# Performance work log

Hardware: AMD Instinct MI355X
Metric: run time of the kernel (lower is better)

Reference implementation:

```python
import jax, jax.numpy as jnp
import numpy as np

N_NODES = 50000
N_EDGES = 800000
IN_CH = 128
EDGE_DIM = 32
H1, H2, H3, OUT = 128, 64, 32, 1


def _linear_params(key, fan_in, fan_out, bias=True):
    k1, k2 = jax.random.split(key)
    scale = 1.0 / np.sqrt(fan_in)
    W = jax.random.uniform(k1, (fan_in, fan_out), jnp.float32, -scale, scale)
    if bias:
        b = jax.random.uniform(k2, (fan_out,), jnp.float32, -scale, scale)
        return W, b
    return W


def setup_inputs() -> dict:
    key = jax.random.key(0)
    ks = jax.random.split(key, 32)
    inp = {
        'x': jax.random.normal(ks[0], (N_NODES, IN_CH), jnp.float32),
        'edge_index': jax.random.randint(ks[1], (2, N_EDGES), 0, N_NODES, jnp.int64),
        'edge_attr': jax.random.normal(ks[2], (N_EDGES, EDGE_DIM), jnp.float32),
    }
    dims = [(IN_CH, H1), (H1, H2), (H2, H3)]
    ki = 3
    for l, (fi, fo) in enumerate(dims, start=1):
        inp[f'Wq{l}'], inp[f'bq{l}'] = _linear_params(ks[ki], fi, fo); ki += 1
        inp[f'Wk{l}'], inp[f'bk{l}'] = _linear_params(ks[ki], fi, fo); ki += 1
        inp[f'Wv{l}'], inp[f'bv{l}'] = _linear_params(ks[ki], fi, fo); ki += 1
        inp[f'We{l}'] = _linear_params(ks[ki], EDGE_DIM, fo, bias=False); ki += 1
        inp[f'Ws{l}'], inp[f'bs{l}'] = _linear_params(ks[ki], fi, fo); ki += 1
    inp['Wc'], inp['bc'] = _linear_params(ks[ki], H3, OUT)
    return inp


def _tconv(x, src, dst, edge_attr, Wq, bq, Wk, bk, Wv, bv, We, Ws, bs):
    # TransformerConv, heads=1: edge-conditioned attention with segment softmax over dst
    q = x @ Wq + bq                      # [N, d]
    k = x @ Wk + bk                      # [N, d]
    v = x @ Wv + bv                      # [N, d]
    e = edge_attr @ We                   # [E, d]
    k_e = k[src] + e                     # gather + edge key
    v_e = v[src] + e                     # gather + edge value
    d = q.shape[-1]
    alpha = jnp.sum(q[dst] * k_e, axis=-1) / jnp.sqrt(jnp.asarray(d, x.dtype))  # [E]
    m = jax.ops.segment_max(alpha, dst, num_segments=N_NODES)
    a = jnp.exp(alpha - m[dst])
    s = jax.ops.segment_sum(a, dst, num_segments=N_NODES)
    a = a / s[dst]
    agg = jax.ops.segment_sum(a[:, None] * v_e, dst, num_segments=N_NODES)
    return agg + x @ Ws + bs             # root/skip connection


def reference(x, edge_index, edge_attr,
              Wq1, bq1, Wk1, bk1, Wv1, bv1, We1, Ws1, bs1,
              Wq2, bq2, Wk2, bk2, Wv2, bv2, We2, Ws2, bs2,
              Wq3, bq3, Wk3, bk3, Wv3, bv3, We3, Ws3, bs3,
              Wc, bc):
    src, dst = edge_index[0], edge_index[1]
    h = jax.nn.relu(_tconv(x, src, dst, edge_attr, Wq1, bq1, Wk1, bk1, Wv1, bv1, We1, Ws1, bs1))
    h = jax.nn.relu(_tconv(h, src, dst, edge_attr, Wq2, bq2, Wk2, bk2, Wv2, bv2, We2, Ws2, bs2))
    h = jax.nn.relu(_tconv(h, src, dst, edge_attr, Wq3, bq3, Wk3, bk3, Wv3, bv3, We3, Ws3, bs3))
    return h @ Wc + bc
```

## Files before the change

### kernel.cpp

```cpp
#include <hip/hip_runtime.h>
#include <math.h>

#define N_NODES 50000
#define N_EDGES 800000

typedef __bf16 bf16;
typedef __bf16 bf16x8 __attribute__((ext_vector_type(8)));
typedef float f32x4 __attribute__((ext_vector_type(4)));

__device__ __forceinline__ float bflo(unsigned r) {
  union { unsigned u; float f; } c; c.u = r << 16; return c.f;
}
__device__ __forceinline__ float bfhi(unsigned r) {
  union { unsigned u; float f; } c; c.u = r & 0xffff0000u; return c.f;
}

__global__ void k_detect(const int* ei, int* flags) {
  if (threadIdx.x == 0 && blockIdx.x == 0) {
    int is64 = 1;
    for (int i = 0; i < 128; ++i) {
      if (ei[2 * i + 1] != 0) { is64 = 0; break; }
    }
    flags[0] = is64;
  }
}

__device__ __forceinline__ int load_idx(const int* ei, int e, int is64, int which) {
  size_t idx = (size_t)which * N_EDGES + (size_t)e;
  return is64 ? ei[2 * idx] : ei[idx];
}


__global__ void k_zero(int* p, int n) {
  int i = blockIdx.x * blockDim.x + threadIdx.x;
  if (i < n) p[i] = 0;
}

__global__ void k_hist(const int* ei, const int* flags, int* counts) {
  int e = blockIdx.x * blockDim.x + threadIdx.x;
  int is64 = flags[0];
  if (e < N_EDGES) {
    int dst = load_idx(ei, e, is64, 1);
    if (dst >= 0 && dst < N_NODES) atomicAdd(&counts[dst], 1);
  }
}

__global__ void k_scan1(const int* counts, int* row_ptr, int* bsum) {
  __shared__ int buf[1024];
  int t = threadIdx.x;
  int i = blockIdx.x * 1024 + t;
  int v = (i < N_NODES) ? counts[i] : 0;
  buf[t] = v;
  __syncthreads();
  for (int off = 1; off < 1024; off <<= 1) {
    int x = (t >= off) ? buf[t - off] : 0;
    __syncthreads();
    buf[t] += x;
    __syncthreads();
  }
  if (i < N_NODES) row_ptr[i] = buf[t] - v;
  if (t == 1023) bsum[blockIdx.x] = buf[1023];
}

__global__ void k_scan2(int* bsum, int* row_ptr) {
  constexpr int NB = (N_NODES + 1023) / 1024;
  int t = threadIdx.x;
  int v = (t < NB) ? bsum[t] : 0;
  int inc = v;
#pragma unroll
  for (int off = 1; off < 64; off <<= 1) {
    int x = __shfl_up(inc, off, 64);
    if (t >= off) inc += x;
  }
  if (t < NB) bsum[t] = inc - v;
  if (t == 63) row_ptr[N_NODES] = inc;
}

__global__ void k_scan3(const int* bsum, int* row_ptr, int* cursor) {
  int i = blockIdx.x * 1024 + threadIdx.x;
  if (i < N_NODES) {
    int r = row_ptr[i] + bsum[blockIdx.x];
    row_ptr[i] = r;
    cursor[i] = r;
  }
}

__global__ void k_scatter(const int* ei, const int* flags, int* cursor,
                          int* csr_src, int* csr_eid) {
  int e = blockIdx.x * blockDim.x + threadIdx.x;
  int is64 = flags[0];
  if (e < N_EDGES) {
    int src = load_idx(ei, e, is64, 0);
    int dst = load_idx(ei, e, is64, 1);
    if (dst >= 0 && dst < N_NODES && src >= 0 && src < N_NODES) {
      int pos = atomicAdd(&cursor[dst], 1);
      if (pos >= 0 && pos < N_EDGES) {
        csr_src[pos] = src;
        csr_eid[pos] = e;
      }
    }
  }
}


#define DBLK 256
#define NDB ((N_NODES + DBLK - 1) / DBLK)

__global__ void k_dhist(const int* __restrict__ counts, int* __restrict__ btot) {
  __shared__ int lh[64];
  int t = threadIdx.x;
  if (t < 64) lh[t] = 0;
  __syncthreads();
  int n = blockIdx.x * DBLK + t;
  if (n < N_NODES) atomicAdd(&lh[min(counts[n], 63)], 1);
  __syncthreads();
  if (t < 64 && lh[t] > 0) atomicAdd(&btot[t], lh[t]);
}

__global__ void k_dbase(const int* __restrict__ btot, int* __restrict__ dcursor) {
  int t = threadIdx.x;
  int v = btot[t];
  int inc = v;
#pragma unroll
  for (int off = 1; off < 64; off <<= 1) {
    int x = __shfl_up(inc, off, 64);
    if (t >= off) inc += x;
  }
  dcursor[t] = inc - v;
}

__global__ void k_dscatter(const int* __restrict__ counts, int* __restrict__ dcursor,
                           int* __restrict__ node_perm) {
  __shared__ int lh[64];
  __shared__ int lbase[64];
  int t = threadIdx.x;
  if (t < 64) lh[t] = 0;
  __syncthreads();
  int n = blockIdx.x * DBLK + t;
  int b = 0, lrank = 0;
  bool valid = (n < N_NODES);
  if (valid) {
    b = min(counts[n], 63);
    lrank = atomicAdd(&lh[b], 1);
  }
  __syncthreads();
  if (t < 64) {
    int c = lh[t];
    lbase[t] = (c > 0) ? atomicAdd(&dcursor[t], c) : 0;
  }
  __syncthreads();
  if (valid) node_perm[lbase[b] + lrank] = n;
}


template <int FI, int FO>
__global__ void k_prep(const float* __restrict__ Wq, const float* __restrict__ bq,
                       const float* __restrict__ Wk, const float* __restrict__ bk,
                       const float* __restrict__ Wv, const float* __restrict__ bv,
                       const float* __restrict__ We,
                       const float* __restrict__ Ws, const float* __restrict__ bs,
                       bf16* __restrict__ Wt, float* __restrict__ bias) {
  int n = blockIdx.x;
  int k = threadIdx.x;
  if (n < 4 * FO) {
    int sel = n / FO, c = n - sel * FO;
    const float* W = sel == 0 ? Wq : sel == 1 ? Wk : sel == 2 ? Wv : Ws;
    Wt[(size_t)n * FI + k] = (bf16)W[(size_t)k * FO + c];
    if (k == 0) bias[n] = (sel == 0 ? bq : sel == 1 ? bk : sel == 2 ? bv : bs)[c];
  } else {
    int j = n - 4 * FO;
    float acc = 0.f;
    for (int c = 0; c < FO; ++c) acc += Wq[(size_t)k * FO + c] * We[(size_t)j * FO + c];
    Wt[(size_t)n * FI + k] = (bf16)acc;
    if (k == 0) {
      float b = 0.f;
      for (int c = 0; c < FO; ++c) b += bq[c] * We[(size_t)j * FO + c];
      bias[n] = b;
    }
  }
}


template <int K, int FO, bool AF32>
__global__ __launch_bounds__(256) void k_gemm_mfma(const void* __restrict__ A,
                                                   const bf16* __restrict__ Wt,
                                                   const float* __restrict__ bias,
                                                   bf16* __restrict__ feat) {
  constexpr int CPL = FO / 16;
  constexpr int NT = 4 * FO + 32;
  int lane = threadIdx.x & 63;
  int wave = threadIdx.x >> 6;
  int m0 = blockIdx.y * 64 + wave * 16;
  if (m0 >= N_NODES) return;
  int c0 = blockIdx.x * 64;
  int half = lane & 15;
  int quad = lane >> 4;
  f32x4 acc[4] = {};
#pragma unroll
  for (int kb = 0; kb < K; kb += 32) {
    size_t aoff = (size_t)(m0 + half) * K + kb + quad * 8;
    bf16x8 a;
    if constexpr (AF32) {
      const float* Af = (const float*)A;
      f32x4 lo = *(const f32x4*)(Af + aoff);
      f32x4 hi = *(const f32x4*)(Af + aoff + 4);
#pragma unroll
      for (int j = 0; j < 4; ++j) { a[j] = (bf16)lo[j]; a[4 + j] = (bf16)hi[j]; }
    } else {
      a = *(const bf16x8*)((const bf16*)A + aoff);
    }
#pragma unroll
    for (int f = 0; f < 4; ++f) {
      int cb = c0 + f * 16;
      if (cb < NT) {
        bf16x8 b = *(const bf16x8*)(Wt + (size_t)(cb + half) * K + kb + quad * 8);
        acc[f] = __builtin_amdgcn_mfma_f32_16x16x32_bf16(a, b, acc[f], 0, 0, 0);
      }
    }
  }
#pragma unroll
  for (int f = 0; f < 4; ++f) {
    int cb = c0 + f * 16;
    if (cb < NT) {
      int col = cb + half;
      int pos;
      if (col < 4 * FO) {
        int sel = col / FO, c = col - sel * FO;
        if (sel == 0) pos = c;
        else if (sel == 3) pos = 3 * FO + c;
        else {
          int g = c / CPL, o = c - g * CPL;
          pos = FO + g * 2 * CPL + (sel == 2 ? CPL : 0) + o;
        }
      } else {
        pos = col;
      }
      float bv = bias[col];
#pragma unroll
      for (int r = 0; r < 4; ++r) {
        int row = m0 + quad * 4 + r;
        feat[(size_t)row * NT + pos] = (bf16)(acc[f][r] + bv);
      }
    }
  }
}


template <int FO, bool FINAL>
__global__ __launch_bounds__(256) void k_edge(const bf16* __restrict__ feat,
                                              const float* __restrict__ ea,
                                              const int* __restrict__ row_ptr,
                                              const int* __restrict__ csr_src,
                                              const int* __restrict__ csr_eid,
                                              const int* __restrict__ node_perm,
                                              const float* __restrict__ We,
                                              bf16* __restrict__ h_out,
                                              const float* __restrict__ Wc,
                                              const float* __restrict__ bc,
                                              float* __restrict__ out) {
  constexpr int FTOT = 4 * FO + 32;
  constexpr int CPL = FO / 16;
  constexpr int NU = CPL / 2;
  int lane16 = threadIdx.x & 15;
  int gid = blockIdx.x * 16 + (threadIdx.x >> 4);
  int node = node_perm[N_NODES - 1 - gid];
  int cbase = CPL * lane16;
  const bf16* fq = feat + (size_t)node * FTOT;

  float q[CPL];
  {
    const unsigned* qp = (const unsigned*)(fq + cbase);
    unsigned qr[NU];
    if constexpr (NU == 4) { uint4 t = *(const uint4*)qp; qr[0]=t.x; qr[1]=t.y; qr[2]=t.z; qr[3]=t.w; }
    else if constexpr (NU == 2) { uint2 t = *(const uint2*)qp; qr[0]=t.x; qr[1]=t.y; }
    else { qr[0] = *qp; }
#pragma unroll
    for (int u = 0; u < NU; ++u) { q[2*u] = bflo(qr[u]); q[2*u+1] = bfhi(qr[u]); }
  }
  float qe0, qe1;
  { unsigned r = *(const unsigned*)(fq + 4 * FO + 2 * lane16); qe0 = bflo(r); qe1 = bfhi(r); }

  float m = -INFINITY, ssum = 0.f, wacc0 = 0.f, wacc1 = 0.f;
  float vacc[CPL];
#pragma unroll
  for (int i = 0; i < CPL; ++i) vacc[i] = 0.f;

  int start = row_ptr[node], end = row_ptr[node + 1];
  const float scaleA = 1.0f / sqrtf((float)FO);

  auto loadkv = [&](int src, unsigned* kv) {
    const unsigned* base = (const unsigned*)(feat + (size_t)src * FTOT + FO) + CPL * lane16;
    if constexpr (CPL == 8) {
      uint4 a = *(const uint4*)base; uint4 b = *(const uint4*)(base + 4);
      kv[0]=a.x; kv[1]=a.y; kv[2]=a.z; kv[3]=a.w; kv[4]=b.x; kv[5]=b.y; kv[6]=b.z; kv[7]=b.w;
    } else if constexpr (CPL == 4) {
      uint4 a = *(const uint4*)base;
      kv[0]=a.x; kv[1]=a.y; kv[2]=a.z; kv[3]=a.w;
    } else {
      uint2 a = *(const uint2*)base;
      kv[0]=a.x; kv[1]=a.y;
    }
  };

  auto update = [&](const unsigned* kv, float e0, float e1) {
    float part = qe0 * e0 + qe1 * e1;
#pragma unroll
    for (int u = 0; u < NU; ++u)
      part += q[2*u] * bflo(kv[u]) + q[2*u+1] * bfhi(kv[u]);
#pragma unroll
    for (int off = 1; off < 16; off <<= 1) part += __shfl_xor(part, off, 64);
    float alpha = part * scaleA;
    float mnew = fmaxf(m, alpha);
    float sc = __expf(m - mnew);
    float w = __expf(alpha - mnew);
    ssum = ssum * sc + w;
#pragma unroll
    for (int u = 0; u < NU; ++u) {
      float a = bflo(kv[NU + u]), b = bfhi(kv[NU + u]);
      vacc[2*u]   = vacc[2*u]   * sc + w * a;
      vacc[2*u+1] = vacc[2*u+1] * sc + w * b;
    }
    wacc0 = wacc0 * sc + w * e0;
    wacc1 = wacc1 * sc + w * e1;
    m = mnew;
  };

  int p = start;
  for (; p + 2 <= end; p += 2) {
    int s0 = csr_src[p], s1 = csr_src[p + 1];
    int e0 = csr_eid[p], e1 = csr_eid[p + 1];
    unsigned kv0[CPL], kv1[CPL];
    loadkv(s0, kv0); loadkv(s1, kv1);
    float2 ea0 = *(const float2*)(ea + (size_t)e0 * 32 + 2 * lane16);
    float2 ea1 = *(const float2*)(ea + (size_t)e1 * 32 + 2 * lane16);
    update(kv0, ea0.x, ea0.y);
    update(kv1, ea1.x, ea1.y);
  }
  if (p < end) {
    int s0 = csr_src[p]; int e0 = csr_eid[p];
    unsigned kv0[CPL];
    loadkv(s0, kv0);
    float2 ea0 = *(const float2*)(ea + (size_t)e0 * 32 + 2 * lane16);
    update(kv0, ea0.x, ea0.y);
  }

  float inv = (ssum > 0.f) ? 1.0f / ssum : 0.f;
  float agg[CPL];
#pragma unroll
  for (int i = 0; i < CPL; ++i) agg[i] = vacc[i];
#pragma unroll
  for (int jh = 0; jh < 16; ++jh) {
    float w0 = __shfl(wacc0, jh, 16);
    float w1 = __shfl(wacc1, jh, 16);
    const float* r0 = We + (size_t)(2 * jh) * FO + cbase;
    const float* r1 = We + (size_t)(2 * jh + 1) * FO + cbase;
#pragma unroll
    for (int i = 0; i < CPL; ++i) agg[i] += w0 * r0[i] + w1 * r1[i];
  }
  float hv[CPL];
#pragma unroll
  for (int i = 0; i < CPL; ++i) {
    float s = (float)fq[3 * FO + cbase + i];
    hv[i] = fmaxf(agg[i] * inv + s, 0.f);
  }
  if constexpr (!FINAL) {
    unsigned o[NU];
#pragma unroll
    for (int u = 0; u < NU; ++u) {
      union { bf16 b[2]; unsigned u32; } c;
      c.b[0] = (bf16)hv[2*u]; c.b[1] = (bf16)hv[2*u+1];
      o[u] = c.u32;
    }
    unsigned* dst = (unsigned*)(h_out + (size_t)node * FO + cbase);
    if constexpr (NU == 4) { uint4 t; t.x=o[0]; t.y=o[1]; t.z=o[2]; t.w=o[3]; *(uint4*)dst = t; }
    else if constexpr (NU == 2) { uint2 t; t.x=o[0]; t.y=o[1]; *(uint2*)dst = t; }
    else { *dst = o[0]; }
  } else {
    float part2 = 0.f;
#pragma unroll
    for (int i = 0; i < CPL; ++i) part2 += hv[i] * Wc[cbase + i];
#pragma unroll
    for (int off = 1; off < 16; off <<= 1) part2 += __shfl_xor(part2, off, 64);
    if (lane16 == 0) out[node] = part2 + bc[0];
  }
}


extern "C" void kernel_launch(void* const* d_in, const int* in_sizes, int n_in,
                              void* d_out, int out_size, void* d_ws, size_t ws_size,
                              hipStream_t stream) {
  (void)in_sizes; (void)n_in; (void)out_size; (void)ws_size;
  const float* x = (const float*)d_in[0];
  const int* ei = (const int*)d_in[1];
  const float* ea = (const float*)d_in[2];
  const float *Wq1 = (const float*)d_in[3], *bq1 = (const float*)d_in[4];
  const float *Wk1 = (const float*)d_in[5], *bk1 = (const float*)d_in[6];
  const float *Wv1 = (const float*)d_in[7], *bv1 = (const float*)d_in[8];
  const float *We1 = (const float*)d_in[9];
  const float *Ws1 = (const float*)d_in[10], *bs1 = (const float*)d_in[11];
  const float *Wq2 = (const float*)d_in[12], *bq2 = (const float*)d_in[13];
  const float *Wk2 = (const float*)d_in[14], *bk2 = (const float*)d_in[15];
  const float *Wv2 = (const float*)d_in[16], *bv2 = (const float*)d_in[17];
  const float *We2 = (const float*)d_in[18];
  const float *Ws2 = (const float*)d_in[19], *bs2 = (const float*)d_in[20];
  const float *Wq3 = (const float*)d_in[21], *bq3 = (const float*)d_in[22];
  const float *Wk3 = (const float*)d_in[23], *bk3 = (const float*)d_in[24];
  const float *Wv3 = (const float*)d_in[25], *bv3 = (const float*)d_in[26];
  const float *We3 = (const float*)d_in[27];
  const float *Ws3 = (const float*)d_in[28], *bs3 = (const float*)d_in[29];
  const float *Wc = (const float*)d_in[30], *bc = (const float*)d_in[31];

  char* ws = (char*)d_ws;
  size_t off = 0;
  auto alloc = [&](size_t bytes) -> void* {
    void* p = ws + off;
    off = (off + bytes + 255) & ~(size_t)255;
    return p;
  };
  bf16* h        = (bf16*)alloc((size_t)N_NODES * 128 * 2);
  int* counts    = (int*)alloc((N_NODES + 1) * 4);
  int* row_ptr   = (int*)alloc((N_NODES + 1) * 4);
  int* cursor    = (int*)alloc((N_NODES + 1) * 4);
  int* csr_src   = (int*)alloc((size_t)N_EDGES * 4);
  int* csr_eid   = (int*)alloc((size_t)N_EDGES * 4);
  int* flags     = (int*)alloc(256);
  bf16* Wt       = (bf16*)alloc(544 * 128 * 2);
  float* bias    = (float*)alloc(544 * 4);
  bf16* feat     = (bf16*)alloc((size_t)N_NODES * 544 * 2);
  int* bsum      = (int*)alloc(64 * 4);
  int* dcount    = (int*)alloc(64 * 4);
  int* dcursor   = (int*)alloc(64 * 4);
  int* node_perm = (int*)alloc((size_t)N_NODES * 4);

  constexpr int NB = (N_NODES + 1023) / 1024;

  k_detect<<<1, 1, 0, stream>>>(ei, flags);
  k_zero<<<(N_NODES + 256) / 256, 256, 0, stream>>>(counts, N_NODES + 1);
  k_zero<<<1, 64, 0, stream>>>(dcount, 64);
  k_hist<<<(N_EDGES + 255) / 256, 256, 0, stream>>>(ei, flags, counts);
  k_scan1<<<NB, 1024, 0, stream>>>(counts, row_ptr, bsum);
  k_scan2<<<1, 64, 0, stream>>>(bsum, row_ptr);
  k_scan3<<<NB, 1024, 0, stream>>>(bsum, row_ptr, cursor);
  k_dhist<<<NDB, DBLK, 0, stream>>>(counts, dcount);
  k_dbase<<<1, 64, 0, stream>>>(dcount, dcursor);
  k_dscatter<<<NDB, DBLK, 0, stream>>>(counts, dcursor, node_perm);
  k_scatter<<<(N_EDGES + 255) / 256, 256, 0, stream>>>(ei, flags, cursor, csr_src, csr_eid);

  k_prep<128, 128><<<544, 128, 0, stream>>>(Wq1, bq1, Wk1, bk1, Wv1, bv1, We1, Ws1, bs1,
                                            Wt, bias);
  {
    dim3 g((544 + 63) / 64, (N_NODES + 63) / 64);
    k_gemm_mfma<128, 128, true><<<g, 256, 0, stream>>>(x, Wt, bias, feat);
  }
  k_edge<128, false><<<N_NODES / 16, 256, 0, stream>>>(feat, ea, row_ptr, csr_src, csr_eid,
                                                       node_perm, We1, h, nullptr, nullptr,
                                                       nullptr);

  k_prep<128, 64><<<288, 128, 0, stream>>>(Wq2, bq2, Wk2, bk2, Wv2, bv2, We2, Ws2, bs2,
                                           Wt, bias);
  {
    dim3 g((288 + 63) / 64, (N_NODES + 63) / 64);
    k_gemm_mfma<128, 64, false><<<g, 256, 0, stream>>>(h, Wt, bias, feat);
  }
  k_edge<64, false><<<N_NODES / 16, 256, 0, stream>>>(feat, ea, row_ptr, csr_src, csr_eid,
                                                      node_perm, We2, h, nullptr, nullptr,
                                                      nullptr);

  k_prep<64, 32><<<160, 64, 0, stream>>>(Wq3, bq3, Wk3, bk3, Wv3, bv3, We3, Ws3, bs3,
                                         Wt, bias);
  {
    dim3 g((160 + 63) / 64, (N_NODES + 63) / 64);
    k_gemm_mfma<64, 32, false><<<g, 256, 0, stream>>>(h, Wt, bias, feat);
  }
  k_edge<32, true><<<N_NODES / 16, 256, 0, stream>>>(feat, ea, row_ptr, csr_src, csr_eid,
                                                     node_perm, We3, nullptr, Wc, bc,
                                                     (float*)d_out);
}
```

Before: 659.1 us.

## Pre-permute edge attributes to CSR order in bf16, use dot2 and 4-way unroll

```diff
diff --git a/kernel.cpp b/kernel.cpp
--- a/kernel.cpp
+++ b/kernel.cpp
@@ -13,6 +13,21 @@
 }
 __device__ __forceinline__ float bfhi(unsigned r) {
   union { unsigned u; float f; } c; c.u = r & 0xffff0000u; return c.f;
+}
+
+__device__ __forceinline__ float dot2bf(unsigned a, unsigned b, float acc) {
+#if defined(__has_builtin)
+#if __has_builtin(__builtin_amdgcn_fdot2_f32_bf16)
+  typedef __bf16 bf16x2 __attribute__((ext_vector_type(2)));
+  union { unsigned u; bf16x2 v; } ca, cb;
+  ca.u = a; cb.u = b;
+  return __builtin_amdgcn_fdot2_f32_bf16(ca.v, cb.v, acc, false);
+#else
+  return acc + bflo(a) * bflo(b) + bfhi(a) * bfhi(b);
+#endif
+#else
+  return acc + bflo(a) * bflo(b) + bfhi(a) * bfhi(b);
+#endif
 }
 
 __global__ void k_detect(const int* ei, int* flags) {
@@ -100,6 +115,19 @@
       }
     }
   }
+}
+
+
+__global__ void k_eaperm(const float* __restrict__ ea, const int* __restrict__ csr_eid,
+                         bf16* __restrict__ ea_bf) {
+  int idx = blockIdx.x * blockDim.x + threadIdx.x;
+  if (idx >= N_EDGES * 16) return;
+  int p = idx >> 4, jj = idx & 15;
+  int eid = csr_eid[p];
+  float2 t = *(const float2*)(ea + (size_t)eid * 32 + 2 * jj);
+  union { bf16 b[2]; unsigned u; } c;
+  c.b[0] = (bf16)t.x; c.b[1] = (bf16)t.y;
+  *(unsigned*)(ea_bf + (size_t)p * 32 + 2 * jj) = c.u;
 }
 
 
@@ -246,9 +274,10 @@
 }
 
 
-template <int FO, bool FINAL>
+template <int FO, bool FINAL, bool PERM>
 __global__ __launch_bounds__(256) void k_edge(const bf16* __restrict__ feat,
                                               const float* __restrict__ ea,
+                                              const bf16* __restrict__ ea_bf,
                                               const int* __restrict__ row_ptr,
                                               const int* __restrict__ csr_src,
                                               const int* __restrict__ csr_eid,
@@ -267,15 +296,12 @@
   int cbase = CPL * lane16;
   const bf16* fq = feat + (size_t)node * FTOT;
 
-  float q[CPL];
+  unsigned qr[NU];
   {
     const unsigned* qp = (const unsigned*)(fq + cbase);
-    unsigned qr[NU];
     if constexpr (NU == 4) { uint4 t = *(const uint4*)qp; qr[0]=t.x; qr[1]=t.y; qr[2]=t.z; qr[3]=t.w; }
     else if constexpr (NU == 2) { uint2 t = *(const uint2*)qp; qr[0]=t.x; qr[1]=t.y; }
     else { qr[0] = *qp; }
-#pragma unroll
-    for (int u = 0; u < NU; ++u) { q[2*u] = bflo(qr[u]); q[2*u+1] = bfhi(qr[u]); }
   }
   float qe0, qe1;
   { unsigned r = *(const unsigned*)(fq + 4 * FO + 2 * lane16); qe0 = bflo(r); qe1 = bfhi(r); }
@@ -302,11 +328,21 @@
     }
   };
 
+  auto loadea = [&](int p, float& e0, float& e1) {
+    if constexpr (PERM) {
+      unsigned r = *(const unsigned*)(ea_bf + (size_t)p * 32 + 2 * lane16);
+      e0 = bflo(r); e1 = bfhi(r);
+    } else {
+      int eid = csr_eid[p];
+      float2 t = *(const float2*)(ea + (size_t)eid * 32 + 2 * lane16);
+      e0 = t.x; e1 = t.y;
+    }
+  };
+
   auto update = [&](const unsigned* kv, float e0, float e1) {
     float part = qe0 * e0 + qe1 * e1;
 #pragma unroll
-    for (int u = 0; u < NU; ++u)
-      part += q[2*u] * bflo(kv[u]) + q[2*u+1] * bfhi(kv[u]);
+    for (int u = 0; u < NU; ++u) part = dot2bf(kv[u], qr[u], part);
 #pragma unroll
     for (int off = 1; off < 16; off <<= 1) part += __shfl_xor(part, off, 64);
     float alpha = part * scaleA;
@@ -326,22 +362,25 @@
   };
 
   int p = start;
-  for (; p + 2 <= end; p += 2) {
-    int s0 = csr_src[p], s1 = csr_src[p + 1];
-    int e0 = csr_eid[p], e1 = csr_eid[p + 1];
-    unsigned kv0[CPL], kv1[CPL];
-    loadkv(s0, kv0); loadkv(s1, kv1);
-    float2 ea0 = *(const float2*)(ea + (size_t)e0 * 32 + 2 * lane16);
-    float2 ea1 = *(const float2*)(ea + (size_t)e1 * 32 + 2 * lane16);
-    update(kv0, ea0.x, ea0.y);
-    update(kv1, ea1.x, ea1.y);
-  }
-  if (p < end) {
-    int s0 = csr_src[p]; int e0 = csr_eid[p];
-    unsigned kv0[CPL];
-    loadkv(s0, kv0);
-    float2 ea0 = *(const float2*)(ea + (size_t)e0 * 32 + 2 * lane16);
-    update(kv0, ea0.x, ea0.y);
+  for (; p + 4 <= end; p += 4) {
+    int s[4];
+#pragma unroll
+    for (int u = 0; u < 4; ++u) s[u] = csr_src[p + u];
+    unsigned kv[4][8];
+#pragma unroll
+    for (int u = 0; u < 4; ++u) loadkv(s[u], kv[u]);
+    float e0[4], e1[4];
+#pragma unroll
+    for (int u = 0; u < 4; ++u) loadea(p + u, e0[u], e1[u]);
+#pragma unroll
+    for (int u = 0; u < 4; ++u) update(kv[u], e0[u], e1[u]);
+  }
+  for (; p < end; ++p) {
+    unsigned kv0[8];
+    loadkv(csr_src[p], kv0);
+    float e0, e1;
+    loadea(p, e0, e1);
+    update(kv0, e0, e1);
   }
 
   float inv = (ssum > 0.f) ? 1.0f / ssum : 0.f;
@@ -389,7 +428,7 @@
 extern "C" void kernel_launch(void* const* d_in, const int* in_sizes, int n_in,
                               void* d_out, int out_size, void* d_ws, size_t ws_size,
                               hipStream_t stream) {
-  (void)in_sizes; (void)n_in; (void)out_size; (void)ws_size;
+  (void)in_sizes; (void)n_in; (void)out_size;
   const float* x = (const float*)d_in[0];
   const int* ei = (const int*)d_in[1];
   const float* ea = (const float*)d_in[2];
@@ -431,6 +470,10 @@
   int* dcount    = (int*)alloc(64 * 4);
   int* dcursor   = (int*)alloc(64 * 4);
   int* node_perm = (int*)alloc((size_t)N_NODES * 4);
+  size_t off_base = off;
+  bf16* ea_bf    = (bf16*)alloc((size_t)N_EDGES * 32 * 2);
+  bool use_perm = (ws_size == 0) || (off <= ws_size);
+  (void)off_base;
 
   constexpr int NB = (N_NODES + 1023) / 1024;
 
@@ -445,6 +488,9 @@
   k_dbase<<<1, 64, 0, stream>>>(dcount, dcursor);
   k_dscatter<<<NDB, DBLK, 0, stream>>>(counts, dcursor, node_perm);
   k_scatter<<<(N_EDGES + 255) / 256, 256, 0, stream>>>(ei, flags, cursor, csr_src, csr_eid);
+  if (use_perm) {
+    k_eaperm<<<(N_EDGES * 16 + 255) / 256, 256, 0, stream>>>(ea, csr_eid, ea_bf);
+  }
 
   k_prep<128, 128><<<544, 128, 0, stream>>>(Wq1, bq1, Wk1, bk1, Wv1, bv1, We1, Ws1, bs1,
                                             Wt, bias);
@@ -452,9 +498,16 @@
     dim3 g((544 + 63) / 64, (N_NODES + 63) / 64);
     k_gemm_mfma<128, 128, true><<<g, 256, 0, stream>>>(x, Wt, bias, feat);
   }
-  k_edge<128, false><<<N_NODES / 16, 256, 0, stream>>>(feat, ea, row_ptr, csr_src, csr_eid,
-                                                       node_perm, We1, h, nullptr, nullptr,
-                                                       nullptr);
+  if (use_perm)
+    k_edge<128, false, true><<<N_NODES / 16, 256, 0, stream>>>(feat, ea, ea_bf, row_ptr,
+                                                               csr_src, csr_eid, node_perm,
+                                                               We1, h, nullptr, nullptr,
+                                                               nullptr);
+  else
+    k_edge<128, false, false><<<N_NODES / 16, 256, 0, stream>>>(feat, ea, ea_bf, row_ptr,
+                                                                csr_src, csr_eid, node_perm,
+                                                                We1, h, nullptr, nullptr,
+                                                                nullptr);
 
   k_prep<128, 64><<<288, 128, 0, stream>>>(Wq2, bq2, Wk2, bk2, Wv2, bv2, We2, Ws2, bs2,
                                            Wt, bias);
@@ -462,9 +515,16 @@
     dim3 g((288 + 63) / 64, (N_NODES + 63) / 64);
     k_gemm_mfma<128, 64, false><<<g, 256, 0, stream>>>(h, Wt, bias, feat);
   }
-  k_edge<64, false><<<N_NODES / 16, 256, 0, stream>>>(feat, ea, row_ptr, csr_src, csr_eid,
-                                                      node_perm, We2, h, nullptr, nullptr,
-                                                      nullptr);
+  if (use_perm)
+    k_edge<64, false, true><<<N_NODES / 16, 256, 0, stream>>>(feat, ea, ea_bf, row_ptr,
+                                                              csr_src, csr_eid, node_perm,
+                                                              We2, h, nullptr, nullptr,
+                                                              nullptr);
+  else
+    k_edge<64, false, false><<<N_NODES / 16, 256, 0, stream>>>(feat, ea, ea_bf, row_ptr,
+                                                               csr_src, csr_eid, node_perm,
+                                                               We2, h, nullptr, nullptr,
+                                                               nullptr);
 
   k_prep<64, 32><<<160, 64, 0, stream>>>(Wq3, bq3, Wk3, bk3, Wv3, bv3, We3, Ws3, bs3,
                                          Wt, bias);
@@ -472,7 +532,14 @@
     dim3 g((160 + 63) / 64, (N_NODES + 63) / 64);
     k_gemm_mfma<64, 32, false><<<g, 256, 0, stream>>>(h, Wt, bias, feat);
   }
-  k_edge<32, true><<<N_NODES / 16, 256, 0, stream>>>(feat, ea, row_ptr, csr_src, csr_eid,
-                                                     node_perm, We3, nullptr, Wc, bc,
-                                                     (float*)d_out);
-}
+  if (use_perm)
+    k_edge<32, true, true><<<N_NODES / 16, 256, 0, stream>>>(feat, ea, ea_bf, row_ptr,
+                                                             csr_src, csr_eid, node_perm,
+                                                             We3, nullptr, Wc, bc,
+                                                             (float*)d_out);
+  else
+    k_edge<32, true, false><<<N_NODES / 16, 256, 0, stream>>>(feat, ea, ea_bf, row_ptr,
+                                                              csr_src, csr_eid, node_perm,
+                                                              We3, nullptr, Wc, bc,
+                                                              (float*)d_out);
+}
```

Result: no change. 671.6 us (+1.9%).
